# Optimization experiments

Measured on AMD Instinct MI355X. Metric: run time of the kernel, lower is better.

The kernel has to match this reference:

```python
import jax, jax.numpy as jnp
import numpy as np

NUM_CATEGORIES = 32
INPUT_DIM = 1024
HIDDEN_DIM = 2048
B, T = 64, 256


def setup_inputs() -> dict:
    key = jax.random.key(0)
    k_x, k_cat, k_w = jax.random.split(key, 3)
    x = jax.random.normal(k_x, (B, T, INPUT_DIM), dtype=jnp.float32)
    cat_ids = jax.random.randint(k_cat, (B,), 0, NUM_CATEGORIES, dtype=jnp.int32)
    W = 0.02 * jax.random.normal(k_w, (NUM_CATEGORIES, INPUT_DIM, HIDDEN_DIM), dtype=jnp.float32)
    b = jnp.zeros((NUM_CATEGORIES, HIDDEN_DIM), dtype=jnp.float32)
    return {"x": x, "cat_ids": cat_ids, "W": W, "b": b}


def reference(x, cat_ids, W, b):
    # Gather per-sample weight [B, in, hid] and bias [B, hid], then batched matmul.
    selected_W = W[cat_ids]            # [B, INPUT_DIM, HIDDEN_DIM]
    selected_b = b[cat_ids]            # [B, HIDDEN_DIM]
    out = jnp.einsum('bti,bih->bth', x, selected_W) + selected_b[:, None, :]
    return out
```

## Files before the change

### kernel.cpp

```cpp
#include <hip/hip_runtime.h>
#include <hip/hip_bf16.h>

#define NUM_CAT 32
#define IN_DIM 1024
#define HID_DIM 2048
#define T_DIM 256
#define B_DIM 64

typedef __attribute__((ext_vector_type(4))) float floatx4;
typedef __attribute__((ext_vector_type(8))) short shortx8;

__device__ __forceinline__ unsigned short f2bf(float f) {
  unsigned u = __builtin_bit_cast(unsigned, f);
  u += 0x7FFFu + ((u >> 16) & 1u);
  return (unsigned short)(u >> 16);
}

#define GLDS16(g, l) __builtin_amdgcn_global_load_lds( \
    (const __attribute__((address_space(1))) unsigned int*)(g), \
    (__attribute__((address_space(3))) unsigned int*)(l), 16, 0, 0)

__global__ __launch_bounds__(256) void conv_w_kernel(
    const float* __restrict__ W, unsigned short* __restrict__ Wt) {
  __shared__ unsigned short t[64][66];
  const int ntile = blockIdx.x;
  const int ktile = blockIdx.y;
  const int c     = blockIdx.z;
  const int tid = threadIdx.x;
  const int r  = tid >> 4;
  const int c4 = (tid & 15) * 4;

  const float* src = W + ((size_t)c * IN_DIM + (size_t)ktile * 64) * HID_DIM + (size_t)ntile * 64;
  #pragma unroll
  for (int p = 0; p < 4; ++p) {
    const int k = p * 16 + r;
    const float4 v = *reinterpret_cast<const float4*>(src + (size_t)k * HID_DIM + c4);
    t[k][c4 + 0] = f2bf(v.x);
    t[k][c4 + 1] = f2bf(v.y);
    t[k][c4 + 2] = f2bf(v.z);
    t[k][c4 + 3] = f2bf(v.w);
  }
  __syncthreads();
  unsigned short* dst = Wt + ((size_t)c * HID_DIM + (size_t)ntile * 64) * IN_DIM + (size_t)ktile * 64;
  #pragma unroll
  for (int p = 0; p < 4; ++p) {
    const int n = p * 16 + r;
    ushort4 o;
    o.x = t[c4 + 0][n];
    o.y = t[c4 + 1][n];
    o.z = t[c4 + 2][n];
    o.w = t[c4 + 3][n];
    *reinterpret_cast<ushort4*>(dst + (size_t)n * IN_DIM + c4) = o;
  }
}

__global__ __launch_bounds__(256) void conv_x_kernel(
    const float* __restrict__ x, unsigned short* __restrict__ xb) {
  const int total4 = B_DIM * T_DIM * IN_DIM / 4;
  for (int i = blockIdx.x * blockDim.x + threadIdx.x; i < total4;
       i += gridDim.x * blockDim.x) {
    const float4 v = reinterpret_cast<const float4*>(x)[i];
    ushort4 h;
    h.x = f2bf(v.x); h.y = f2bf(v.y); h.z = f2bf(v.z); h.w = f2bf(v.w);
    reinterpret_cast<ushort4*>(xb)[i] = h;
  }
}

__global__ __launch_bounds__(256) void cat_gemm_bf16_kernel(
    const unsigned short* __restrict__ xb, const int* __restrict__ cat_ids,
    const unsigned short* __restrict__ Wt, const float* __restrict__ bias,
    float* __restrict__ out) {
  const int nt = blockIdx.x;
  const int mt = blockIdx.y;
  const int b  = blockIdx.z;
  const int tid = threadIdx.x;
  const int c = cat_ids[b];

  __shared__ __attribute__((aligned(16))) unsigned short As[128 * 64];
  __shared__ __attribute__((aligned(16))) unsigned short Bs[128 * 64];

  const int lane = tid & 63;
  const int wv   = tid >> 6;
  const int wm   = (wv >> 1) * 64;
  const int wn   = (wv & 1) * 64;
  const int l16  = lane & 15;
  const int quad = lane >> 4;

  const int row_st = tid >> 3;
  const int kb_st  = (tid & 7) * 16;

  const char* xa = (const char*)xb + (size_t)(b * T_DIM + mt * 128) * (IN_DIM * 2);
  const char* wa = (const char*)Wt + ((size_t)c * HID_DIM + (size_t)nt * 128) * (IN_DIM * 2);

  floatx4 acc[4][4] = {};

  for (int ks = 0; ks < IN_DIM / 64; ++ks) {
    const size_t kbase = (size_t)ks * 128;

    #pragma unroll
    for (int i = 0; i < 4; ++i) {
      const int m  = i * 32 + row_st;
      const int kb = kb_st ^ ((m & 7) << 4);
      GLDS16(xa + (size_t)m * 2048 + kbase + kb, (char*)As + i * 4096 + tid * 16);
      GLDS16(wa + (size_t)m * 2048 + kbase + kb, (char*)Bs + i * 4096 + tid * 16);
    }

    __syncthreads();

    shortx8 af[4][2], bfr[4][2];
    #pragma unroll
    for (int i = 0; i < 4; ++i) {
      const int row = wm + i * 16 + l16;
      const int sw  = (row & 7) << 4;
      af[i][0] = *reinterpret_cast<const shortx8*>((const char*)As + row * 128 + ((quad * 16) ^ sw));
      af[i][1] = *reinterpret_cast<const shortx8*>((const char*)As + row * 128 + ((64 + quad * 16) ^ sw));
    }
    #pragma unroll
    for (int j = 0; j < 4; ++j) {
      const int row = wn + j * 16 + l16;
      const int sw  = (row & 7) << 4;
      bfr[j][0] = *reinterpret_cast<const shortx8*>((const char*)Bs + row * 128 + ((quad * 16) ^ sw));
      bfr[j][1] = *reinterpret_cast<const shortx8*>((const char*)Bs + row * 128 + ((64 + quad * 16) ^ sw));
    }

    #pragma unroll
    for (int s = 0; s < 2; ++s)
      #pragma unroll
      for (int i = 0; i < 4; ++i)
        #pragma unroll
        for (int j = 0; j < 4; ++j)
          acc[i][j] = __builtin_amdgcn_mfma_f32_16x16x32_bf16(af[i][s], bfr[j][s], acc[i][j], 0, 0, 0);

    __syncthreads();
  }

  float* outp = out + ((size_t)b * T_DIM + (size_t)mt * 128) * HID_DIM + nt * 128;
  const float* bp = bias + (size_t)c * HID_DIM + nt * 128;
  #pragma unroll
  for (int j = 0; j < 4; ++j) {
    const float bj = bp[wn + j * 16 + l16];
    #pragma unroll
    for (int i = 0; i < 4; ++i) {
      #pragma unroll
      for (int r = 0; r < 4; ++r) {
        const int m = wm + i * 16 + quad * 4 + r;
        outp[(size_t)m * HID_DIM + wn + j * 16 + l16] = acc[i][j][r] + bj;
      }
    }
  }
}

__global__ __launch_bounds__(256) void cat_linear_fallback_kernel(
    const float* __restrict__ x, const int* __restrict__ cat_ids,
    const float* __restrict__ W, const float* __restrict__ bias,
    float* __restrict__ out) {
  const int nt = blockIdx.x;
  const int mt = blockIdx.y;
  const int b  = blockIdx.z;
  const int tid = threadIdx.x;
  const int c = cat_ids[b];

  const int n0 = nt * 128;
  const float* xbp = x + ((size_t)b * T_DIM + (size_t)mt * 128) * IN_DIM;
  const float* Wc = W + (size_t)c * IN_DIM * HID_DIM + n0;

  __shared__ __attribute__((aligned(16))) unsigned short As[128 * 32];
  __shared__ __attribute__((aligned(16))) unsigned short Bs[128 * 40];

  const int lane = tid & 63;
  const int wv   = tid >> 6;
  const int wm   = (wv >> 1) * 64;
  const int wn   = (wv & 1) * 64;
  const int l16  = lane & 15;
  const int quad = lane >> 4;

  floatx4 acc[4][4] = {};

  const int ar = tid >> 3;
  const int ac = (tid & 7) * 4;
  const int kp = tid >> 4;
  const int bn = (tid & 15) * 4;

  for (int ks = 0; ks < IN_DIM / 32; ++ks) {
    const int k0 = ks * 32;
    #pragma unroll
    for (int p = 0; p < 4; ++p) {
      const int m = ar + p * 32;
      const float4 v = *reinterpret_cast<const float4*>(xbp + (size_t)m * IN_DIM + k0 + ac);
      ushort4 h;
      h.x = f2bf(v.x); h.y = f2bf(v.y); h.z = f2bf(v.z); h.w = f2bf(v.w);
      *reinterpret_cast<ushort4*>(&As[m * 32 + ac]) = h;
    }
    #pragma unroll
    for (int q = 0; q < 2; ++q) {
      const int n = bn + q * 64;
      const float4 v0 = *reinterpret_cast<const float4*>(Wc + (size_t)(k0 + 2 * kp)     * HID_DIM + n);
      const float4 v1 = *reinterpret_cast<const float4*>(Wc + (size_t)(k0 + 2 * kp + 1) * HID_DIM + n);
      unsigned w;
      w = (unsigned)f2bf(v0.x) | ((unsigned)f2bf(v1.x) << 16);
      *reinterpret_cast<unsigned*>(&Bs[(n + 0) * 40 + 2 * kp]) = w;
      w = (unsigned)f2bf(v0.y) | ((unsigned)f2bf(v1.y) << 16);
      *reinterpret_cast<unsigned*>(&Bs[(n + 1) * 40 + 2 * kp]) = w;
      w = (unsigned)f2bf(v0.z) | ((unsigned)f2bf(v1.z) << 16);
      *reinterpret_cast<unsigned*>(&Bs[(n + 2) * 40 + 2 * kp]) = w;
      w = (unsigned)f2bf(v0.w) | ((unsigned)f2bf(v1.w) << 16);
      *reinterpret_cast<unsigned*>(&Bs[(n + 3) * 40 + 2 * kp]) = w;
    }
    __syncthreads();

    shortx8 af[4], bfr[4];
    #pragma unroll
    for (int i = 0; i < 4; ++i)
      af[i] = *reinterpret_cast<const shortx8*>(&As[(wm + i * 16 + l16) * 32 + quad * 8]);
    #pragma unroll
    for (int j = 0; j < 4; ++j)
      bfr[j] = *reinterpret_cast<const shortx8*>(&Bs[(wn + j * 16 + l16) * 40 + quad * 8]);

    #pragma unroll
    for (int i = 0; i < 4; ++i)
      #pragma unroll
      for (int j = 0; j < 4; ++j)
        acc[i][j] = __builtin_amdgcn_mfma_f32_16x16x32_bf16(af[i], bfr[j], acc[i][j], 0, 0, 0);

    __syncthreads();
  }

  float* outp = out + ((size_t)b * T_DIM + (size_t)mt * 128) * HID_DIM + n0;
  const float* bp = bias + (size_t)c * HID_DIM + n0;
  #pragma unroll
  for (int j = 0; j < 4; ++j) {
    const float bj = bp[wn + j * 16 + l16];
    #pragma unroll
    for (int i = 0; i < 4; ++i) {
      #pragma unroll
      for (int r = 0; r < 4; ++r) {
        const int m = wm + i * 16 + quad * 4 + r;
        outp[(size_t)m * HID_DIM + wn + j * 16 + l16] = acc[i][j][r] + bj;
      }
    }
  }
}

extern "C" void kernel_launch(void* const* d_in, const int* in_sizes, int n_in,
                              void* d_out, int out_size, void* d_ws, size_t ws_size,
                              hipStream_t stream) {
  const float* x    = (const float*)d_in[0];
  const int*   cat  = (const int*)d_in[1];
  const float* W    = (const float*)d_in[2];
  const float* bias = (const float*)d_in[3];
  float* out = (float*)d_out;

  const size_t WT_BYTES = (size_t)NUM_CAT * HID_DIM * IN_DIM * 2;
  const size_t XB_BYTES = (size_t)B_DIM * T_DIM * IN_DIM * 2;

  if (ws_size >= WT_BYTES + XB_BYTES) {
    unsigned short* Wt  = (unsigned short*)d_ws;
    unsigned short* xbf = (unsigned short*)((char*)d_ws + WT_BYTES);

    hipLaunchKernelGGL(conv_w_kernel, dim3(HID_DIM / 64, IN_DIM / 64, NUM_CAT),
                       dim3(256), 0, stream, W, Wt);
    hipLaunchKernelGGL(conv_x_kernel, dim3(2048), dim3(256), 0, stream, x, xbf);

    hipLaunchKernelGGL(cat_gemm_bf16_kernel, dim3(HID_DIM / 128, T_DIM / 128, B_DIM),
                       dim3(256), 0, stream, xbf, cat, Wt, bias, out);
  } else {
    hipLaunchKernelGGL(cat_linear_fallback_kernel,
                       dim3(HID_DIM / 128, T_DIM / 128, B_DIM), dim3(256), 0, stream,
                       x, cat, W, bias, out);
  }
}
```

Before: 564.6 us.

## Fuse fp32-to-bf16 conversion into the GEMM and drop pre-conversion kernels

Removes the separate kernels that converted all 32 weight matrices (most of them unused) and x to bf16 in workspace. The conversion and transpose now happen inside the GEMM as each fp32 tile is loaded from global memory into swizzled LDS. This avoids converting unused categories and the extra global write and re-read. The cost is that the GEMM now loads fp32 (twice the bytes) through registers instead of async global-to-LDS loads, and each weight tile is converted again by every block that uses it.

After: 548.0 us. 2.9% less time.

```diff
diff --git a/kernel.cpp b/kernel.cpp
--- a/kernel.cpp
+++ b/kernel.cpp
@@ -16,59 +16,13 @@
   return (unsigned short)(u >> 16);
 }
 
-#define GLDS16(g, l) __builtin_amdgcn_global_load_lds( \
-    (const __attribute__((address_space(1))) unsigned int*)(g), \
-    (__attribute__((address_space(3))) unsigned int*)(l), 16, 0, 0)
-
-__global__ __launch_bounds__(256) void conv_w_kernel(
-    const float* __restrict__ W, unsigned short* __restrict__ Wt) {
-  __shared__ unsigned short t[64][66];
-  const int ntile = blockIdx.x;
-  const int ktile = blockIdx.y;
-  const int c     = blockIdx.z;
-  const int tid = threadIdx.x;
-  const int r  = tid >> 4;
-  const int c4 = (tid & 15) * 4;
-
-  const float* src = W + ((size_t)c * IN_DIM + (size_t)ktile * 64) * HID_DIM + (size_t)ntile * 64;
-  #pragma unroll
-  for (int p = 0; p < 4; ++p) {
-    const int k = p * 16 + r;
-    const float4 v = *reinterpret_cast<const float4*>(src + (size_t)k * HID_DIM + c4);
-    t[k][c4 + 0] = f2bf(v.x);
-    t[k][c4 + 1] = f2bf(v.y);
-    t[k][c4 + 2] = f2bf(v.z);
-    t[k][c4 + 3] = f2bf(v.w);
-  }
-  __syncthreads();
-  unsigned short* dst = Wt + ((size_t)c * HID_DIM + (size_t)ntile * 64) * IN_DIM + (size_t)ktile * 64;
-  #pragma unroll
-  for (int p = 0; p < 4; ++p) {
-    const int n = p * 16 + r;
-    ushort4 o;
-    o.x = t[c4 + 0][n];
-    o.y = t[c4 + 1][n];
-    o.z = t[c4 + 2][n];
-    o.w = t[c4 + 3][n];
-    *reinterpret_cast<ushort4*>(dst + (size_t)n * IN_DIM + c4) = o;
-  }
+__device__ __forceinline__ unsigned pack2(float a, float b) {
+  return (unsigned)f2bf(a) | ((unsigned)f2bf(b) << 16);
 }
 
-__global__ __launch_bounds__(256) void conv_x_kernel(
-    const float* __restrict__ x, unsigned short* __restrict__ xb) {
-  const int total4 = B_DIM * T_DIM * IN_DIM / 4;
-  for (int i = blockIdx.x * blockDim.x + threadIdx.x; i < total4;
-       i += gridDim.x * blockDim.x) {
-    const float4 v = reinterpret_cast<const float4*>(x)[i];
-    ushort4 h;
-    h.x = f2bf(v.x); h.y = f2bf(v.y); h.z = f2bf(v.z); h.w = f2bf(v.w);
-    reinterpret_cast<ushort4*>(xb)[i] = h;
-  }
-}
-
-__global__ __launch_bounds__(256) void cat_gemm_bf16_kernel(
-    const unsigned short* __restrict__ xb, const int* __restrict__ cat_ids,
-    const unsigned short* __restrict__ Wt, const float* __restrict__ bias,
+__global__ __launch_bounds__(256) void cat_linear_fused_kernel(
+    const float* __restrict__ x, const int* __restrict__ cat_ids,
+    const float* __restrict__ W, const float* __restrict__ bias,
     float* __restrict__ out) {
   const int nt = blockIdx.x;
   const int mt = blockIdx.y;
@@ -86,147 +40,94 @@
   const int l16  = lane & 15;
   const int quad = lane >> 4;
 
-  const int row_st = tid >> 3;
-  const int kb_st  = (tid & 7) * 16;
+  const int ar = tid >> 3;
+  const int au = tid & 7;
+  const int bn4 = (tid & 31) * 4;
+  const int bk8 = (tid >> 5) * 8;
 
-  const char* xa = (const char*)xb + (size_t)(b * T_DIM + mt * 128) * (IN_DIM * 2);
-  const char* wa = (const char*)Wt + ((size_t)c * HID_DIM + (size_t)nt * 128) * (IN_DIM * 2);
+  const float* xb = x + ((size_t)b * T_DIM + (size_t)mt * 128) * IN_DIM;
+  const float* Wc = W + (size_t)c * IN_DIM * HID_DIM + (size_t)nt * 128;
 
   floatx4 acc[4][4] = {};
 
   for (int ks = 0; ks < IN_DIM / 64; ++ks) {
-    const size_t kbase = (size_t)ks * 128;
+    const int k0 = ks * 64;
 
     #pragma unroll
     for (int i = 0; i < 4; ++i) {
-      const int m  = i * 32 + row_st;
-      const int kb = kb_st ^ ((m & 7) << 4);
-      GLDS16(xa + (size_t)m * 2048 + kbase + kb, (char*)As + i * 4096 + tid * 16);
-      GLDS16(wa + (size_t)m * 2048 + kbase + kb, (char*)Bs + i * 4096 + tid * 16);
+      const int m = i * 32 + ar;
+      const float* ap = xb + (size_t)m * IN_DIM + k0 + au * 8;
+      const float4 v0 = *reinterpret_cast<const float4*>(ap);
+      const float4 v1 = *reinterpret_cast<const float4*>(ap + 4);
+      union { shortx8 s8; unsigned u[4]; } pk;
+      pk.u[0] = pack2(v0.x, v0.y);
+      pk.u[1] = pack2(v0.z, v0.w);
+      pk.u[2] = pack2(v1.x, v1.y);
+      pk.u[3] = pack2(v1.z, v1.w);
+      *reinterpret_cast<shortx8*>(
+          (char*)As + m * 128 + ((au * 16) ^ ((m & 7) << 4))) = pk.s8;
+    }
+
+    {
+      const float* wp = Wc + (size_t)(k0 + bk8) * HID_DIM + bn4;
+      const float4 w0 = *reinterpret_cast<const float4*>(wp + 0 * HID_DIM);
+      const float4 w1 = *reinterpret_cast<const float4*>(wp + 1 * HID_DIM);
+      const float4 w2 = *reinterpret_cast<const float4*>(wp + 2 * HID_DIM);
+      const float4 w3 = *reinterpret_cast<const float4*>(wp + 3 * HID_DIM);
+      const float4 w4 = *reinterpret_cast<const float4*>(wp + 4 * HID_DIM);
+      const float4 w5 = *reinterpret_cast<const float4*>(wp + 5 * HID_DIM);
+      const float4 w6 = *reinterpret_cast<const float4*>(wp + 6 * HID_DIM);
+      const float4 w7 = *reinterpret_cast<const float4*>(wp + 7 * HID_DIM);
+      union { shortx8 s8; unsigned u[4]; } pk;
+      pk.u[0] = pack2(w0.x, w1.x); pk.u[1] = pack2(w2.x, w3.x);
+      pk.u[2] = pack2(w4.x, w5.x); pk.u[3] = pack2(w6.x, w7.x);
+      *reinterpret_cast<shortx8*>(
+          (char*)Bs + (bn4 + 0) * 128 + ((bk8 * 2) ^ (((bn4 + 0) & 7) << 4))) = pk.s8;
+      pk.u[0] = pack2(w0.y, w1.y); pk.u[1] = pack2(w2.y, w3.y);
+      pk.u[2] = pack2(w4.y, w5.y); pk.u[3] = pack2(w6.y, w7.y);
+      *reinterpret_cast<shortx8*>(
+          (char*)Bs + (bn4 + 1) * 128 + ((bk8 * 2) ^ (((bn4 + 1) & 7) << 4))) = pk.s8;
+      pk.u[0] = pack2(w0.z, w1.z); pk.u[1] = pack2(w2.z, w3.z);
+      pk.u[2] = pack2(w4.z, w5.z); pk.u[3] = pack2(w6.z, w7.z);
+      *reinterpret_cast<shortx8*>(
+          (char*)Bs + (bn4 + 2) * 128 + ((bk8 * 2) ^ (((bn4 + 2) & 7) << 4))) = pk.s8;
+      pk.u[0] = pack2(w0.w, w1.w); pk.u[1] = pack2(w2.w, w3.w);
+      pk.u[2] = pack2(w4.w, w5.w); pk.u[3] = pack2(w6.w, w7.w);
+      *reinterpret_cast<shortx8*>(
+          (char*)Bs + (bn4 + 3) * 128 + ((bk8 * 2) ^ (((bn4 + 3) & 7) << 4))) = pk.s8;
     }
 
     __syncthreads();
 
-    shortx8 af[4][2], bfr[4][2];
     #pragma unroll
-    for (int i = 0; i < 4; ++i) {
-      const int row = wm + i * 16 + l16;
-      const int sw  = (row & 7) << 4;
-      af[i][0] = *reinterpret_cast<const shortx8*>((const char*)As + row * 128 + ((quad * 16) ^ sw));
-      af[i][1] = *reinterpret_cast<const shortx8*>((const char*)As + row * 128 + ((64 + quad * 16) ^ sw));
-    }
-    #pragma unroll
-    for (int j = 0; j < 4; ++j) {
-      const int row = wn + j * 16 + l16;
-      const int sw  = (row & 7) << 4;
-      bfr[j][0] = *reinterpret_cast<const shortx8*>((const char*)Bs + row * 128 + ((quad * 16) ^ sw));
-      bfr[j][1] = *reinterpret_cast<const shortx8*>((const char*)Bs + row * 128 + ((64 + quad * 16) ^ sw));
-    }
-
-    #pragma unroll
-    for (int s = 0; s < 2; ++s)
+    for (int s = 0; s < 2; ++s) {
+      shortx8 af[4], bfr[4];
+      #pragma unroll
+      for (int i = 0; i < 4; ++i) {
+        const int row = wm + i * 16 + l16;
+        const int sw  = (row & 7) << 4;
+        af[i] = *reinterpret_cast<const shortx8*>(
+            (const char*)As + row * 128 + ((s * 64 + quad * 16) ^ sw));
+      }
+      #pragma unroll
+      for (int j = 0; j < 4; ++j) {
+        const int row = wn + j * 16 + l16;
+        const int sw  = (row & 7) << 4;
+        bfr[j] = *reinterpret_cast<const shortx8*>(
+            (const char*)Bs + row * 128 + ((s * 64 + quad * 16) ^ sw));
+      }
       #pragma unroll
       for (int i = 0; i < 4; ++i)
         #pragma unroll
         for (int j = 0; j < 4; ++j)
-          acc[i][j] = __builtin_amdgcn_mfma_f32_16x16x32_bf16(af[i][s], bfr[j][s], acc[i][j], 0, 0, 0);
+          acc[i][j] = __builtin_amdgcn_mfma_f32_16x16x32_bf16(af[i], bfr[j], acc[i][j], 0, 0, 0);
+    }
 
     __syncthreads();
   }
 
   float* outp = out + ((size_t)b * T_DIM + (size_t)mt * 128) * HID_DIM + nt * 128;
   const float* bp = bias + (size_t)c * HID_DIM + nt * 128;
-  #pragma unroll
-  for (int j = 0; j < 4; ++j) {
-    const float bj = bp[wn + j * 16 + l16];
-    #pragma unroll
-    for (int i = 0; i < 4; ++i) {
-      #pragma unroll
-      for (int r = 0; r < 4; ++r) {
-        const int m = wm + i * 16 + quad * 4 + r;
-        outp[(size_t)m * HID_DIM + wn + j * 16 + l16] = acc[i][j][r] + bj;
-      }
-    }
-  }
-}
-
-__global__ __launch_bounds__(256) void cat_linear_fallback_kernel(
-    const float* __restrict__ x, const int* __restrict__ cat_ids,
-    const float* __restrict__ W, const float* __restrict__ bias,
-    float* __restrict__ out) {
-  const int nt = blockIdx.x;
-  const int mt = blockIdx.y;
-  const int b  = blockIdx.z;
-  const int tid = threadIdx.x;
-  const int c = cat_ids[b];
-
-  const int n0 = nt * 128;
-  const float* xbp = x + ((size_t)b * T_DIM + (size_t)mt * 128) * IN_DIM;
-  const float* Wc = W + (size_t)c * IN_DIM * HID_DIM + n0;
-
-  __shared__ __attribute__((aligned(16))) unsigned short As[128 * 32];
-  __shared__ __attribute__((aligned(16))) unsigned short Bs[128 * 40];
-
-  const int lane = tid & 63;
-  const int wv   = tid >> 6;
-  const int wm   = (wv >> 1) * 64;
-  const int wn   = (wv & 1) * 64;
-  const int l16  = lane & 15;
-  const int quad = lane >> 4;
-
-  floatx4 acc[4][4] = {};
-
-  const int ar = tid >> 3;
-  const int ac = (tid & 7) * 4;
-  const int kp = tid >> 4;
-  const int bn = (tid & 15) * 4;
-
-  for (int ks = 0; ks < IN_DIM / 32; ++ks) {
-    const int k0 = ks * 32;
-    #pragma unroll
-    for (int p = 0; p < 4; ++p) {
-      const int m = ar + p * 32;
-      const float4 v = *reinterpret_cast<const float4*>(xbp + (size_t)m * IN_DIM + k0 + ac);
-      ushort4 h;
-      h.x = f2bf(v.x); h.y = f2bf(v.y); h.z = f2bf(v.z); h.w = f2bf(v.w);
-      *reinterpret_cast<ushort4*>(&As[m * 32 + ac]) = h;
-    }
-    #pragma unroll
-    for (int q = 0; q < 2; ++q) {
-      const int n = bn + q * 64;
-      const float4 v0 = *reinterpret_cast<const float4*>(Wc + (size_t)(k0 + 2 * kp)     * HID_DIM + n);
-      const float4 v1 = *reinterpret_cast<const float4*>(Wc + (size_t)(k0 + 2 * kp + 1) * HID_DIM + n);
-      unsigned w;
-      w = (unsigned)f2bf(v0.x) | ((unsigned)f2bf(v1.x) << 16);
-      *reinterpret_cast<unsigned*>(&Bs[(n + 0) * 40 + 2 * kp]) = w;
-      w = (unsigned)f2bf(v0.y) | ((unsigned)f2bf(v1.y) << 16);
-      *reinterpret_cast<unsigned*>(&Bs[(n + 1) * 40 + 2 * kp]) = w;
-      w = (unsigned)f2bf(v0.z) | ((unsigned)f2bf(v1.z) << 16);
-      *reinterpret_cast<unsigned*>(&Bs[(n + 2) * 40 + 2 * kp]) = w;
-      w = (unsigned)f2bf(v0.w) | ((unsigned)f2bf(v1.w) << 16);
-      *reinterpret_cast<unsigned*>(&Bs[(n + 3) * 40 + 2 * kp]) = w;
-    }
-    __syncthreads();
-
-    shortx8 af[4], bfr[4];
-    #pragma unroll
-    for (int i = 0; i < 4; ++i)
-      af[i] = *reinterpret_cast<const shortx8*>(&As[(wm + i * 16 + l16) * 32 + quad * 8]);
-    #pragma unroll
-    for (int j = 0; j < 4; ++j)
-      bfr[j] = *reinterpret_cast<const shortx8*>(&Bs[(wn + j * 16 + l16) * 40 + quad * 8]);
-
-    #pragma unroll
-    for (int i = 0; i < 4; ++i)
-      #pragma unroll
-      for (int j = 0; j < 4; ++j)
-        acc[i][j] = __builtin_amdgcn_mfma_f32_16x16x32_bf16(af[i], bfr[j], acc[i][j], 0, 0, 0);
-
-    __syncthreads();
-  }
-
-  float* outp = out + ((size_t)b * T_DIM + (size_t)mt * 128) * HID_DIM + n0;
-  const float* bp = bias + (size_t)c * HID_DIM + n0;
   #pragma unroll
   for (int j = 0; j < 4; ++j) {
     const float bj = bp[wn + j * 16 + l16];
@@ -250,22 +151,7 @@
   const float* bias = (const float*)d_in[3];
   float* out = (float*)d_out;
 
-  const size_t WT_BYTES = (size_t)NUM_CAT * HID_DIM * IN_DIM * 2;
-  const size_t XB_BYTES = (size_t)B_DIM * T_DIM * IN_DIM * 2;
-
-  if (ws_size >= WT_BYTES + XB_BYTES) {
-    unsigned short* Wt  = (unsigned short*)d_ws;
-    unsigned short* xbf = (unsigned short*)((char*)d_ws + WT_BYTES);
-
-    hipLaunchKernelGGL(conv_w_kernel, dim3(HID_DIM / 64, IN_DIM / 64, NUM_CAT),
-                       dim3(256), 0, stream, W, Wt);
-    hipLaunchKernelGGL(conv_x_kernel, dim3(2048), dim3(256), 0, stream, x, xbf);
-
-    hipLaunchKernelGGL(cat_gemm_bf16_kernel, dim3(HID_DIM / 128, T_DIM / 128, B_DIM),
-                       dim3(256), 0, stream, xbf, cat, Wt, bias, out);
-  } else {
-    hipLaunchKernelGGL(cat_linear_fallback_kernel,
-                       dim3(HID_DIM / 128, T_DIM / 128, B_DIM), dim3(256), 0, stream,
-                       x, cat, W, bias, out);
-  }
+  dim3 grid(HID_DIM / 128, T_DIM / 128, B_DIM);
+  hipLaunchKernelGGL(cat_linear_fused_kernel, grid, dim3(256), 0, stream,
+                     x, cat, W, bias, out);
 }
```
